# Optimization experiments

Measured on AMD Instinct MI355X. Metric: run time of the kernel, lower is better.

Reference implementation:

```python
import jax, jax.numpy as jnp
import numpy as np

SIGMA2 = 0.01       # inlier_params[0] -> Scorer_dist sigma2
INLIER_ALPHA = 0.5  # inlier_params[-1]


def setup_inputs() -> dict:
    key = jax.random.key(0)
    k1, k2, k3 = jax.random.split(key, 3)
    B, H, N = 32, 256, 8192
    pts = jax.random.normal(k1, (B, N, 3), dtype=jnp.float32)
    target = jax.random.normal(k2, (B, 3), dtype=jnp.float32)
    sample_idx = jax.random.randint(k3, (B, H, 3), 0, N)
    return {"pts": pts, "target": target, "sample_idx": sample_idx}


def _fit_planes(pts, sample_idx):
    # gather 3 points per hypothesis: pts [B,N,3], sample_idx [B,H,3] -> [B,H,3,3]
    B = pts.shape[0]
    b_idx = jnp.arange(B)[:, None, None]
    tri = pts[b_idx, sample_idx]                     # [B,H,3pts,3coords]
    p0, p1, p2 = tri[:, :, 0], tri[:, :, 1], tri[:, :, 2]
    n = jnp.cross(p1 - p0, p2 - p0)                  # plane normal [B,H,3]
    d = -jnp.sum(n * p0, axis=-1, keepdims=True)     # plane offset [B,H,1]
    planes = jnp.concatenate([n, d], axis=-1)        # [B,H,4]
    # sample_hyp fallback: degenerate (all-zero) planes replaced by ones
    all_zero = jnp.all(planes == 0, axis=-1, keepdims=True)
    planes = jnp.where(all_zero, jnp.ones_like(planes), planes)
    # normalize all 4 components by normal norm
    norm = jnp.sqrt(jnp.sum(planes[..., :3] ** 2, axis=-1, keepdims=True))
    return planes / norm


def reference(pts, target, sample_idx):
    B = pts.shape[0]
    planes = _fit_planes(pts, sample_idx)            # [B,H,4]
    normal = planes[..., :3]
    # Scorer_dist: |n . p + d| over all points, gaussian, sum over points
    dists = jnp.abs(jnp.einsum('bhc,bnc->bhn', normal, pts) + planes[..., 3:4])
    score = jnp.sum(jnp.exp(-(dists ** 2) / (2.0 * SIGMA2)), axis=2)  # [B,H]
    # ms_euclidean loss against target normal (sign-invariant)
    t = target[:, None, :]                           # [B,1,3]
    loss = jnp.minimum(jnp.sum((normal - t) ** 2, axis=2),
                       jnp.sum((normal + t) ** 2, axis=2))            # [B,H]
    maxidx = jnp.argmax(score, axis=1)               # [B]
    top_loss = jnp.take_along_axis(loss, maxidx[:, None], axis=1)[:, 0]
    pred = jnp.take_along_axis(normal, maxidx[:, None, None], axis=1)[:, 0]
    w = jax.nn.softmax(INLIER_ALPHA * score, axis=1)
    exp_loss = jnp.sum(loss * w, axis=1)             # [B]
    return exp_loss, top_loss, pred
```

## Files before the change

### kernel.cpp

```cpp
#include <hip/hip_runtime.h>
#include <math.h>

#define BB 32
#define HH 256
#define NN 8192
#define CC 32
#define CHUNK (NN / CC)
#define P 8
#define SUB (CHUNK / P)


__global__ __launch_bounds__(64) void fit_planes_kernel(
    const float* __restrict__ pts, const float* __restrict__ target,
    const int* __restrict__ sidx, float* __restrict__ ws) {
  int b = blockIdx.y;
  int h = blockIdx.x * 64 + threadIdx.x;
  long base = ((long)b * HH + h) * 3;
  int i0 = sidx[base + 0], i1 = sidx[base + 1], i2 = sidx[base + 2];
  const float* pb = pts + (long)b * NN * 3;
  float p0x = pb[3 * i0], p0y = pb[3 * i0 + 1], p0z = pb[3 * i0 + 2];
  float p1x = pb[3 * i1], p1y = pb[3 * i1 + 1], p1z = pb[3 * i1 + 2];
  float p2x = pb[3 * i2], p2y = pb[3 * i2 + 1], p2z = pb[3 * i2 + 2];
  float v1x = p1x - p0x, v1y = p1y - p0y, v1z = p1z - p0z;
  float v2x = p2x - p0x, v2y = p2y - p0y, v2z = p2z - p0z;
  float nx = __fsub_rn(__fmul_rn(v1y, v2z), __fmul_rn(v1z, v2y));
  float ny = __fsub_rn(__fmul_rn(v1z, v2x), __fmul_rn(v1x, v2z));
  float nz = __fsub_rn(__fmul_rn(v1x, v2y), __fmul_rn(v1y, v2x));
  float d = -(__fmul_rn(nx, p0x) + __fmul_rn(ny, p0y) + __fmul_rn(nz, p0z));
  if (nx == 0.0f && ny == 0.0f && nz == 0.0f && d == 0.0f) {
    nx = 1.0f; ny = 1.0f; nz = 1.0f; d = 1.0f;
  }
  float norm = sqrtf(nx * nx + ny * ny + nz * nz);
  nx /= norm; ny /= norm; nz /= norm; d /= norm;
  ((float4*)ws)[b * HH + h] = make_float4(nx, ny, nz, d);
  float tx = target[b * 3], ty = target[b * 3 + 1], tz = target[b * 3 + 2];
  float lm = (nx - tx) * (nx - tx) + (ny - ty) * (ny - ty) + (nz - tz) * (nz - tz);
  float lp = (nx + tx) * (nx + tx) + (ny + ty) * (ny + ty) + (nz + tz) * (nz + tz);
  ws[(size_t)BB * HH * 4 + b * HH + h] = fminf(lm, lp);
}

__global__ __launch_bounds__(HH) void score_kernel(
    const float* __restrict__ pts, const float* __restrict__ ws,
    float* __restrict__ partial) {
  const int chunk = blockIdx.x, b = blockIdx.y;
  const int h = threadIdx.x;
  __shared__ float4 smp[CHUNK * 3 / 4];
  __shared__ float scorepad[HH * 9];

  const float4* src4 =
      (const float4*)(pts + ((long)b * NN + (long)chunk * CHUNK) * 3);
  if (h < CHUNK * 3 / 4) {
    __builtin_amdgcn_global_load_lds(src4 + h, &smp[h], 16, 0, 0);
  }

  const float SC = 8.4932180028801371f;
  const int pid = h & 31;
  const int s = h >> 5;
  float4 pls[P];
#pragma unroll
  for (int k = 0; k < P; ++k) {
    float4 q = ((const float4*)ws)[b * HH + pid + (k << 5)];
    pls[k] = make_float4(q.x * SC, q.y * SC, q.z * SC, q.w * SC);
  }
  __syncthreads();

  float acc[P];
#pragma unroll
  for (int k = 0; k < P; ++k) acc[k] = 0.f;
  const int sbase = s * (SUB * 3 / 4);
#pragma unroll 2
  for (int g = 0; g < SUB / 4; ++g) {
    float4 v0 = smp[sbase + 3 * g + 0];
    float4 v1 = smp[sbase + 3 * g + 1];
    float4 v2 = smp[sbase + 3 * g + 2];
#pragma unroll
    for (int k = 0; k < P; ++k) {
      float4 q = pls[k];
      float t0 = fmaf(q.x, v0.x, fmaf(q.y, v0.y, fmaf(q.z, v0.z, q.w)));
      float t1 = fmaf(q.x, v0.w, fmaf(q.y, v1.x, fmaf(q.z, v1.y, q.w)));
      float t2 = fmaf(q.x, v1.z, fmaf(q.y, v1.w, fmaf(q.z, v2.x, q.w)));
      float t3 = fmaf(q.x, v2.y, fmaf(q.y, v2.z, fmaf(q.z, v2.w, q.w)));
      float e0 = __builtin_amdgcn_exp2f(-(t0 * t0));
      float e1 = __builtin_amdgcn_exp2f(-(t1 * t1));
      float e2 = __builtin_amdgcn_exp2f(-(t2 * t2));
      float e3 = __builtin_amdgcn_exp2f(-(t3 * t3));
      acc[k] += (e0 + e1) + (e2 + e3);
    }
  }

#pragma unroll
  for (int k = 0; k < P; ++k) scorepad[(pid + (k << 5)) * 9 + s] = acc[k];
  __syncthreads();
  float rowsum = 0.f;
#pragma unroll
  for (int j = 0; j < P; ++j) rowsum += scorepad[h * 9 + j];
  partial[((long)b * CC + chunk) * HH + h] = rowsum;
}

__global__ __launch_bounds__(HH) void finalize_kernel(
    const float* __restrict__ ws, float* __restrict__ out) {
  int b = blockIdx.x, h = threadIdx.x;
  const float* lossArr = ws + (size_t)BB * HH * 4;
  const float* partial = ws + (size_t)BB * HH * 5;
  float s = 0.f;
#pragma unroll
  for (int c = 0; c < CC; ++c) s += partial[((long)b * CC + c) * HH + h];
  float l = lossArr[b * HH + h];

  __shared__ float sv[HH];
  __shared__ int si[HH];
  __shared__ float s1[HH];
  __shared__ float s2[HH];
  sv[h] = s; si[h] = h;
  __syncthreads();
  for (int off = HH / 2; off > 0; off >>= 1) {
    if (h < off) {
      float o = sv[h + off]; int oi = si[h + off];
      if (o > sv[h] || (o == sv[h] && oi < si[h])) { sv[h] = o; si[h] = oi; }
    }
    __syncthreads();
  }
  float m = sv[0];
  int mi = si[0];
  __syncthreads();
  const float HL = 0.72134752044448170f;
  float wv = __builtin_amdgcn_exp2f(HL * (s - m));
  s1[h] = wv; s2[h] = wv * l;
  __syncthreads();
  for (int off = HH / 2; off > 0; off >>= 1) {
    if (h < off) { s1[h] += s1[h + off]; s2[h] += s2[h + off]; }
    __syncthreads();
  }
  if (h == 0) {
    out[b] = s2[0] / s1[0];
    out[BB + b] = lossArr[b * HH + mi];
    float4 p = ((const float4*)ws)[b * HH + mi];
    out[2 * BB + b * 3 + 0] = p.x;
    out[2 * BB + b * 3 + 1] = p.y;
    out[2 * BB + b * 3 + 2] = p.z;
  }
}

extern "C" void kernel_launch(void* const* d_in, const int* in_sizes, int n_in,
                              void* d_out, int out_size, void* d_ws, size_t ws_size,
                              hipStream_t stream) {
  const float* pts = (const float*)d_in[0];
  const float* target = (const float*)d_in[1];
  const int* sidx = (const int*)d_in[2];
  float* out = (float*)d_out;
  float* ws = (float*)d_ws;
  float* partial = ws + (size_t)BB * HH * 5;

  fit_planes_kernel<<<dim3(HH / 64, BB), 64, 0, stream>>>(pts, target, sidx, ws);
  score_kernel<<<dim3(CC, BB), HH, 0, stream>>>(pts, ws, partial);
  finalize_kernel<<<BB, HH, 0, stream>>>(ws, out);
}
```

Measured before the change: 26.45 us.

## Fuse finalize into score kernel via last-block atomic counter, halve chunk count

```diff
diff --git a/kernel.cpp b/kernel.cpp
--- a/kernel.cpp
+++ b/kernel.cpp
@@ -4,17 +4,21 @@
 #define BB 32
 #define HH 256
 #define NN 8192
-#define CC 32
+#define CC 16
 #define CHUNK (NN / CC)
 #define P 8
 #define SUB (CHUNK / P)
 
+#define WS_LOSS_F   ((size_t)BB * HH * 4)
+#define WS_CNT_F    (WS_LOSS_F + BB * HH)
+#define WS_PART_F   (WS_CNT_F + 64)
 
 __global__ __launch_bounds__(64) void fit_planes_kernel(
     const float* __restrict__ pts, const float* __restrict__ target,
-    const int* __restrict__ sidx, float* __restrict__ ws) {
+    const int* __restrict__ sidx, float* __restrict__ ws, int* __restrict__ cnt) {
   int b = blockIdx.y;
   int h = blockIdx.x * 64 + threadIdx.x;
+  if (blockIdx.x == 0 && threadIdx.x == 0) cnt[b] = 0;
   long base = ((long)b * HH + h) * 3;
   int i0 = sidx[base + 0], i1 = sidx[base + 1], i2 = sidx[base + 2];
   const float* pb = pts + (long)b * NN * 3;
@@ -36,21 +40,26 @@
   float tx = target[b * 3], ty = target[b * 3 + 1], tz = target[b * 3 + 2];
   float lm = (nx - tx) * (nx - tx) + (ny - ty) * (ny - ty) + (nz - tz) * (nz - tz);
   float lp = (nx + tx) * (nx + tx) + (ny + ty) * (ny + ty) + (nz + tz) * (nz + tz);
-  ws[(size_t)BB * HH * 4 + b * HH + h] = fminf(lm, lp);
+  ws[WS_LOSS_F + b * HH + h] = fminf(lm, lp);
 }
 
-__global__ __launch_bounds__(HH) void score_kernel(
+__global__ __launch_bounds__(HH) void score_finalize_kernel(
     const float* __restrict__ pts, const float* __restrict__ ws,
-    float* __restrict__ partial) {
+    float* __restrict__ partial, int* __restrict__ cnt, float* __restrict__ out) {
   const int chunk = blockIdx.x, b = blockIdx.y;
   const int h = threadIdx.x;
   __shared__ float4 smp[CHUNK * 3 / 4];
   __shared__ float scorepad[HH * 9];
+  __shared__ float sv[HH];
+  __shared__ int si[HH];
+  __shared__ float s1[HH];
+  __shared__ float s2[HH];
+  __shared__ int isLast;
 
   const float4* src4 =
       (const float4*)(pts + ((long)b * NN + (long)chunk * CHUNK) * 3);
-  if (h < CHUNK * 3 / 4) {
-    __builtin_amdgcn_global_load_lds(src4 + h, &smp[h], 16, 0, 0);
+  for (int j = h; j < CHUNK * 3 / 4; j += HH) {
+    __builtin_amdgcn_global_load_lds(src4 + j, &smp[j], 16, 0, 0);
   }
 
   const float SC = 8.4932180028801371f;
@@ -95,23 +104,25 @@
 #pragma unroll
   for (int j = 0; j < P; ++j) rowsum += scorepad[h * 9 + j];
   partial[((long)b * CC + chunk) * HH + h] = rowsum;
-}
 
-__global__ __launch_bounds__(HH) void finalize_kernel(
-    const float* __restrict__ ws, float* __restrict__ out) {
-  int b = blockIdx.x, h = threadIdx.x;
-  const float* lossArr = ws + (size_t)BB * HH * 4;
-  const float* partial = ws + (size_t)BB * HH * 5;
-  float s = 0.f;
+  __threadfence();
+  __syncthreads();
+  if (h == 0) {
+    int old = atomicAdd(&cnt[b], 1);
+    isLast = (old == CC - 1) ? 1 : 0;
+  }
+  __syncthreads();
+  if (!isLast) return;
+  __threadfence();
+
+  const float* lossArr = ws + WS_LOSS_F;
+  const float* prow = partial + (long)b * CC * HH + h;
+  float score = 0.f;
 #pragma unroll
-  for (int c = 0; c < CC; ++c) s += partial[((long)b * CC + c) * HH + h];
+  for (int c = 0; c < CC; ++c) score += prow[(long)c * HH];
   float l = lossArr[b * HH + h];
 
-  __shared__ float sv[HH];
-  __shared__ int si[HH];
-  __shared__ float s1[HH];
-  __shared__ float s2[HH];
-  sv[h] = s; si[h] = h;
+  sv[h] = score; si[h] = h;
   __syncthreads();
   for (int off = HH / 2; off > 0; off >>= 1) {
     if (h < off) {
@@ -124,7 +135,7 @@
   int mi = si[0];
   __syncthreads();
   const float HL = 0.72134752044448170f;
-  float wv = __builtin_amdgcn_exp2f(HL * (s - m));
+  float wv = __builtin_amdgcn_exp2f(HL * (score - m));
   s1[h] = wv; s2[h] = wv * l;
   __syncthreads();
   for (int off = HH / 2; off > 0; off >>= 1) {
@@ -149,9 +160,9 @@
   const int* sidx = (const int*)d_in[2];
   float* out = (float*)d_out;
   float* ws = (float*)d_ws;
-  float* partial = ws + (size_t)BB * HH * 5;
+  int* cnt = (int*)(ws + WS_CNT_F);
+  float* partial = ws + WS_PART_F;
 
-  fit_planes_kernel<<<dim3(HH / 64, BB), 64, 0, stream>>>(pts, target, sidx, ws);
-  score_kernel<<<dim3(CC, BB), HH, 0, stream>>>(pts, ws, partial);
-  finalize_kernel<<<BB, HH, 0, stream>>>(ws, out);
+  fit_planes_kernel<<<dim3(HH / 64, BB), 64, 0, stream>>>(pts, target, sidx, ws, cnt);
+  score_finalize_kernel<<<dim3(CC, BB), HH, 0, stream>>>(pts, ws, partial, cnt, out);
 }
```

Result: slower. 62.04 us (+134.6%).
